# Performance work log

Measured on AMD Instinct MI355X. Metric: run time of the kernel, lower is better.

## Reference

```python
import jax, jax.numpy as jnp
import numpy as np

BN_EPS = 1e-5


def setup_inputs() -> dict:
    N, E, IND, HID = 50000, 800000, 128, 64
    key = jax.random.key(0)
    ks = jax.random.split(key, 4)
    x = jax.random.normal(ks[0], (N, IND), dtype=jnp.float32)
    edge_index = jax.random.randint(ks[1], (2, E), 0, N, dtype=jnp.int64)
    edge_attr = jax.random.normal(ks[2], (E, 1), dtype=jnp.float32)
    # Linear(indim, hiddendim, bias=False): weight [HID, IND]
    W = jax.random.normal(ks[3], (HID, IND), dtype=jnp.float32) * (1.0 / np.sqrt(IND))
    bias = jnp.zeros((HID,), dtype=jnp.float32)
    gamma = jnp.ones((HID,), dtype=jnp.float32)
    beta = jnp.zeros((HID,), dtype=jnp.float32)
    return {"x": x, "edge_index": edge_index, "edge_attr": edge_attr,
            "W": W, "bias": bias, "gamma": gamma, "beta": beta}


def reference(x, edge_index, edge_attr, W, bias, gamma, beta):
    N = x.shape[0]
    # add_self_loops
    loop = jnp.arange(N, dtype=edge_index.dtype)
    row = jnp.concatenate([edge_index[0], loop])  # source nodes
    col = jnp.concatenate([edge_index[1], loop])  # target nodes
    # linear (no bias)
    h = x @ W.T  # [N, HID]
    # symmetric GCN normalization: deg computed over col (targets)
    deg = jax.ops.segment_sum(jnp.ones_like(col, dtype=h.dtype), col, num_segments=N)
    deg_inv_sqrt = jnp.where(deg > 0, jax.lax.rsqrt(jnp.maximum(deg, 1.0)), 0.0)
    norm = deg_inv_sqrt[row] * deg_inv_sqrt[col]  # [E+N]
    # gather-scale-scatter: message x_j = h[row], aggregate (add) at col
    msg = norm[:, None] * h[row]                   # [E+N, HID]
    out = jax.ops.segment_sum(msg, col, num_segments=N)  # [N, HID]
    out = jax.nn.relu(out + bias)
    # BatchNorm1d (training mode: batch statistics, biased variance)
    mean = out.mean(axis=0)
    var = out.var(axis=0)
    return gamma * (out - mean) * jax.lax.rsqrt(var + BN_EPS) + beta
```

## Files before the change

kernel.cpp:

```cpp
#include <hip/hip_runtime.h>

constexpr int IND = 128;
constexpr int HID = 64;
constexpr int STRIDE = 64;
constexpr int BSHIFT = 7;
constexpr int BNODES = 128;
constexpr int NBMAX = 512;
constexpr int BCAP = 2560;
constexpr int CH = 4096;
constexpr int EPT = CH / 256;
constexpr int GB = 2048;
constexpr int RB = 64;
constexpr float BN_EPS = 1e-5f;

static inline size_t align256(size_t x) { return (x + 255) & ~(size_t)255; }

__device__ inline ushort f2bf(float f) {
  uint u = __float_as_uint(f);
  uint r = (u + 0x7FFFu + ((u >> 16) & 1u)) >> 16;
  return (ushort)r;
}
__device__ inline float bf2f(ushort u) {
  return __uint_as_float(((uint)u) << 16);
}

__global__ __launch_bounds__(256) void k_init(int* __restrict__ gCursor,
                                              int* __restrict__ cnt,
                                              uint* __restrict__ hrow, int N) {
  int i = threadIdx.x;
  gCursor[i] = 0;
  gCursor[i + 256] = 0;
  if (i == 0) cnt[N] = 0;
  if (i < 32) hrow[i] = 0;
}

__global__ __launch_bounds__(256) void k_fusedA(
    const float* __restrict__ x, const float* __restrict__ W,
    const int* __restrict__ col, const int* __restrict__ row,
    int* __restrict__ gCursor, uint* __restrict__ gBuf,
    ushort* __restrict__ h, int N, int E, int PARTB) {
  __shared__ float ws[IND * HID];
  int tid = threadIdx.x;
  if ((int)blockIdx.x < PARTB) {
    int* hist = (int*)ws;
    int* gbase = hist + NBMAX;
    for (int i = tid; i < NBMAX; i += 256) hist[i] = 0;
    __syncthreads();
    uint pay_[EPT];
    int b_[EPT];
    int r_[EPT];
    int bs = blockIdx.x * CH;
    const int4* col4 = (const int4*)(col + bs);
    const int4* row4 = (const int4*)(row + bs);
    int rem = E - bs;
#pragma unroll
    for (int j = 0; j < EPT / 4; ++j) {
      int i4 = j * 256 + tid;
      int base = i4 << 2;
      if (base < rem) {
        int4 c = col4[i4];
        int4 r = row4[i4];
        int cc[4] = {c.x, c.y, c.z, c.w};
        int rr[4] = {r.x, r.y, r.z, r.w};
#pragma unroll
        for (int t = 0; t < 4; ++t) {
          int jj = j * 4 + t;
          if (base + t < rem) {
            int b = cc[t] >> BSHIFT;
            b_[jj] = b;
            pay_[jj] = ((uint)(cc[t] & (BNODES - 1)) << 16) | (uint)rr[t];
            r_[jj] = atomicAdd(&hist[b], 1);
          } else {
            b_[jj] = -1;
          }
        }
      } else {
#pragma unroll
        for (int t = 0; t < 4; ++t) b_[j * 4 + t] = -1;
      }
    }
    __syncthreads();
    for (int i = tid; i < NBMAX; i += 256) {
      int hcnt = hist[i];
      gbase[i] = (hcnt > 0) ? atomicAdd(&gCursor[i], hcnt) : 0;
    }
    __syncthreads();
#pragma unroll
    for (int j = 0; j < EPT; ++j) {
      if (b_[j] >= 0) {
        int pos = gbase[b_[j]] + r_[j];
        if (pos >= 0 && pos < BCAP) gBuf[(size_t)b_[j] * BCAP + pos] = pay_[j];
      }
    }
  } else {
    int nb = (blockIdx.x - PARTB) * 64;
    for (int id = tid; id < 2048; id += 256) {
      int c = id & 63;
      int k4 = (id >> 6) << 2;
      float4 w = *(const float4*)&W[c * IND + k4];
      ws[(k4 + 0) * HID + c] = w.x;
      ws[(k4 + 1) * HID + c] = w.y;
      ws[(k4 + 2) * HID + c] = w.z;
      ws[(k4 + 3) * HID + c] = w.w;
    }
    __syncthreads();
    const int c0 = (tid & 15) << 2;
    const int n0 = (tid >> 4) << 2;
    const float* xr[4];
#pragma unroll
    for (int j = 0; j < 4; ++j) {
      int node = nb + n0 + j;
      if (node > N - 1) node = N - 1;
      xr[j] = x + (size_t)node * IND;
    }
    float acc[4][4] = {};
    for (int k = 0; k < IND; k += 4) {
      float4 xv0 = *(const float4*)(xr[0] + k);
      float4 xv1 = *(const float4*)(xr[1] + k);
      float4 xv2 = *(const float4*)(xr[2] + k);
      float4 xv3 = *(const float4*)(xr[3] + k);
      float4 w0 = *(const float4*)&ws[(k + 0) * HID + c0];
      float4 w1 = *(const float4*)&ws[(k + 1) * HID + c0];
      float4 w2 = *(const float4*)&ws[(k + 2) * HID + c0];
      float4 w3 = *(const float4*)&ws[(k + 3) * HID + c0];
      acc[0][0] += xv0.x * w0.x + xv0.y * w1.x + xv0.z * w2.x + xv0.w * w3.x;
      acc[0][1] += xv0.x * w0.y + xv0.y * w1.y + xv0.z * w2.y + xv0.w * w3.y;
      acc[0][2] += xv0.x * w0.z + xv0.y * w1.z + xv0.z * w2.z + xv0.w * w3.z;
      acc[0][3] += xv0.x * w0.w + xv0.y * w1.w + xv0.z * w2.w + xv0.w * w3.w;
      acc[1][0] += xv1.x * w0.x + xv1.y * w1.x + xv1.z * w2.x + xv1.w * w3.x;
      acc[1][1] += xv1.x * w0.y + xv1.y * w1.y + xv1.z * w2.y + xv1.w * w3.y;
      acc[1][2] += xv1.x * w0.z + xv1.y * w1.z + xv1.z * w2.z + xv1.w * w3.z;
      acc[1][3] += xv1.x * w0.w + xv1.y * w1.w + xv1.z * w2.w + xv1.w * w3.w;
      acc[2][0] += xv2.x * w0.x + xv2.y * w1.x + xv2.z * w2.x + xv2.w * w3.x;
      acc[2][1] += xv2.x * w0.y + xv2.y * w1.y + xv2.z * w2.y + xv2.w * w3.y;
      acc[2][2] += xv2.x * w0.z + xv2.y * w1.z + xv2.z * w2.z + xv2.w * w3.z;
      acc[2][3] += xv2.x * w0.w + xv2.y * w1.w + xv2.z * w2.w + xv2.w * w3.w;
      acc[3][0] += xv3.x * w0.x + xv3.y * w1.x + xv3.z * w2.x + xv3.w * w3.x;
      acc[3][1] += xv3.x * w0.y + xv3.y * w1.y + xv3.z * w2.y + xv3.w * w3.y;
      acc[3][2] += xv3.x * w0.z + xv3.y * w1.z + xv3.z * w2.z + xv3.w * w3.z;
      acc[3][3] += xv3.x * w0.w + xv3.y * w1.w + xv3.z * w2.w + xv3.w * w3.w;
    }
#pragma unroll
    for (int j = 0; j < 4; ++j) {
      int node = nb + n0 + j;
      if (node < N) {
        ushort4 o;
        o.x = f2bf(acc[j][0]);
        o.y = f2bf(acc[j][1]);
        o.z = f2bf(acc[j][2]);
        o.w = f2bf(acc[j][3]);
        *(ushort4*)&h[(size_t)node * HID + c0] = o;
      }
    }
  }
}

__global__ __launch_bounds__(256) void k_place2(const int* __restrict__ gCursor,
                                                const uint* __restrict__ gBuf,
                                                int* __restrict__ cnt,
                                                ushort* __restrict__ pack,
                                                ushort* __restrict__ h, int N,
                                                uint dummy) {
  __shared__ ushort spack[BNODES * STRIDE];
  __shared__ int scnt[BNODES];
  int tid = threadIdx.x;
  int b = blockIdx.x;
  int node0 = b << BSHIFT;
  uint dd = dummy | (dummy << 16);
  uint4 dv = make_uint4(dd, dd, dd, dd);
  uint4* sp4 = (uint4*)spack;
  for (int i = tid; i < BNODES * STRIDE / 8; i += 256) sp4[i] = dv;
  if (tid < BNODES) scnt[tid] = 0;
  __syncthreads();
  int m = gCursor[b];
  if (m > BCAP) m = BCAP;
  if (m < 0) m = 0;
  const uint* gb = gBuf + (size_t)b * BCAP;
  for (int i = tid; i < m; i += 256) {
    uint pay = gb[i];
    int dL = (int)(pay >> 16);
    ushort src = (ushort)(pay & 0xFFFFu);
    int k = atomicAdd(&scnt[dL], 1);
    if (k < STRIDE) spack[(dL << 6) + k] = src;
  }
  __syncthreads();
  int lim = N - node0;
  if (lim > BNODES) lim = BNODES;
  if (lim <= 0) return;
  uint4* gp4 = (uint4*)(pack + ((size_t)node0 << 6));
  int n4 = lim * (STRIDE / 8);
  for (int i = tid; i < n4; i += 256) gp4[i] = sp4[i];
  for (int j = tid; j < lim; j += 256) cnt[node0 + j] = scnt[j];
  uint4* h4 = (uint4*)(h + ((size_t)node0 << 6));
  int hn = lim * 8;
  for (int i = tid; i < hn; i += 256) {
    int node = i >> 3;
    float dis = rsqrtf((float)scnt[node] + 1.0f);
    uint4 v = h4[i];
    uint r0 = (uint)f2bf(dis * bf2f((ushort)(v.x & 0xffff))) |
              ((uint)f2bf(dis * bf2f((ushort)(v.x >> 16))) << 16);
    uint r1 = (uint)f2bf(dis * bf2f((ushort)(v.y & 0xffff))) |
              ((uint)f2bf(dis * bf2f((ushort)(v.y >> 16))) << 16);
    uint r2 = (uint)f2bf(dis * bf2f((ushort)(v.z & 0xffff))) |
              ((uint)f2bf(dis * bf2f((ushort)(v.z >> 16))) << 16);
    uint r3 = (uint)f2bf(dis * bf2f((ushort)(v.w & 0xffff))) |
              ((uint)f2bf(dis * bf2f((ushort)(v.w >> 16))) << 16);
    h4[i] = make_uint4(r0, r1, r2, r3);
  }
}

__global__ __launch_bounds__(256) void k_gather(const int* __restrict__ cnt,
                                                const ushort* __restrict__ pack,
                                                const ushort* __restrict__ h,
                                                const float* __restrict__ bias,
                                                ushort* __restrict__ ybf,
                                                float* __restrict__ partials,
                                                int N) {
  __shared__ float ls[4][64];
  __shared__ float lq[4][64];
  int tid = threadIdx.x;
  int lane = tid & 63;
  int wv = tid >> 6;
  int gw = blockIdx.x * 4 + wv;
  const int GW = GB * 4;
  float bs = bias[lane];
  float sacc = 0.f, qacc = 0.f;
  for (int wid = gw; wid < N; wid += GW) {
    int cw = __builtin_amdgcn_readfirstlane(cnt[wid]);
    int deg = cw < STRIDE ? cw : STRIDE;
    int pend = (deg + 7) & ~7;
    const ushort* pk = pack + ((size_t)wid << 6);
    float dc = rsqrtf((float)cw + 1.0f);
    float a0 = bf2f(h[(size_t)wid * HID + lane]);
    float a1 = 0.f, a2 = 0.f, a3 = 0.f;
    for (int j = 0; j < pend; j += 8) {
      uint4 pv = *(const uint4*)&pk[j];
      int s0 = (int)(pv.x & 0xffffu), s1 = (int)(pv.x >> 16);
      int s2 = (int)(pv.y & 0xffffu), s3 = (int)(pv.y >> 16);
      int s4 = (int)(pv.z & 0xffffu), s5 = (int)(pv.z >> 16);
      int s6 = (int)(pv.w & 0xffffu), s7 = (int)(pv.w >> 16);
      a0 += bf2f(h[(size_t)s0 * HID + lane]);
      a1 += bf2f(h[(size_t)s1 * HID + lane]);
      a2 += bf2f(h[(size_t)s2 * HID + lane]);
      a3 += bf2f(h[(size_t)s3 * HID + lane]);
      a0 += bf2f(h[(size_t)s4 * HID + lane]);
      a1 += bf2f(h[(size_t)s5 * HID + lane]);
      a2 += bf2f(h[(size_t)s6 * HID + lane]);
      a3 += bf2f(h[(size_t)s7 * HID + lane]);
    }
    float acc = (a0 + a1) + (a2 + a3);
    float y = fmaxf(dc * acc + bs, 0.f);
    ushort yb = f2bf(y);
    ybf[(size_t)wid * HID + lane] = yb;
    float yr = bf2f(yb);
    sacc += yr;
    qacc += yr * yr;
  }
  ls[wv][lane] = sacc;
  lq[wv][lane] = qacc;
  __syncthreads();
  if (tid < 64) {
    float ss = ls[0][tid] + ls[1][tid] + ls[2][tid] + ls[3][tid];
    float qq = lq[0][tid] + lq[1][tid] + lq[2][tid] + lq[3][tid];
    partials[blockIdx.x * 128 + tid] = ss;
    partials[blockIdx.x * 128 + 64 + tid] = qq;
  }
}

__global__ __launch_bounds__(256) void k_reduce(const float* __restrict__ partials,
                                                float* __restrict__ red1) {
  __shared__ float tmp[256];
  int tid = threadIdx.x;
  int c = tid & 127;
  int half = tid >> 7;
  const int PER = GB / RB;
  const int hb = PER / 2;
  int base = blockIdx.x * PER + half * hb;
  float s = 0.f;
  for (int b = base; b < base + hb; ++b) s += partials[b * 128 + c];
  tmp[tid] = s;
  __syncthreads();
  if (tid < 128) red1[blockIdx.x * 128 + tid] = tmp[tid] + tmp[tid + 128];
}

__global__ __launch_bounds__(256) void k_finalize(const ushort* __restrict__ y,
                                                  const float* __restrict__ red1,
                                                  const float* __restrict__ gamma,
                                                  const float* __restrict__ beta,
                                                  float* __restrict__ out,
                                                  float invN, int total8) {
  __shared__ float tmp[256];
  __shared__ float red[128];
  int tid = threadIdx.x;
  {
    int c = tid & 127;
    int half = tid >> 7;
    const int hb = RB / 2;
    float s = 0.f;
    for (int b = half * hb; b < (half + 1) * hb; ++b) s += red1[b * 128 + c];
    tmp[tid] = s;
    __syncthreads();
    if (tid < 128) red[tid] = tmp[tid] + tmp[tid + 128];
    __syncthreads();
  }
  int c0 = (tid & 7) << 3;
  float sc[8], sh[8];
#pragma unroll
  for (int k = 0; k < 8; ++k) {
    int c = c0 + k;
    float mean = red[c] * invN;
    float var = red[64 + c] * invN - mean * mean;
    float istd = rsqrtf(var + BN_EPS);
    float gm = gamma[c] * istd;
    sc[k] = gm;
    sh[k] = beta[c] - mean * gm;
  }
  int start = blockIdx.x * 256 + tid;
  int stride = gridDim.x * 256;
  for (int i = start; i < total8; i += stride) {
    uint4 v = *(const uint4*)&y[(size_t)i * 8];
    float f0 = bf2f((ushort)(v.x & 0xffff)), f1 = bf2f((ushort)(v.x >> 16));
    float f2 = bf2f((ushort)(v.y & 0xffff)), f3 = bf2f((ushort)(v.y >> 16));
    float f4 = bf2f((ushort)(v.z & 0xffff)), f5 = bf2f((ushort)(v.z >> 16));
    float f6 = bf2f((ushort)(v.w & 0xffff)), f7 = bf2f((ushort)(v.w >> 16));
    float4 o0 = make_float4(f0 * sc[0] + sh[0], f1 * sc[1] + sh[1],
                            f2 * sc[2] + sh[2], f3 * sc[3] + sh[3]);
    float4 o1 = make_float4(f4 * sc[4] + sh[4], f5 * sc[5] + sh[5],
                            f6 * sc[6] + sh[6], f7 * sc[7] + sh[7]);
    *(float4*)&out[(size_t)i * 8] = o0;
    *(float4*)&out[(size_t)i * 8 + 4] = o1;
  }
}

extern "C" void kernel_launch(void* const* d_in, const int* in_sizes, int n_in,
                              void* d_out, int out_size, void* d_ws, size_t ws_size,
                              hipStream_t stream) {
  const float* x = (const float*)d_in[0];
  const int* ei = (const int*)d_in[1];
  const float* W = (const float*)d_in[3];
  const float* bias = (const float*)d_in[4];
  const float* gamma = (const float*)d_in[5];
  const float* beta = (const float*)d_in[6];
  const int N = in_sizes[0] / IND;
  const int E = in_sizes[1] / 2;
  const int* rowp = ei;
  const int* colp = ei + E;
  float* out = (float*)d_out;

  const int NBUCK = (N + BNODES - 1) / BNODES;

  char* wsb = (char*)d_ws;
  size_t off = 0;
  int* cnt = (int*)(wsb + off);          off = align256(off + (size_t)(N + 1) * 4);
  int* gCursor = (int*)(wsb + off);      off = align256(off + (size_t)NBMAX * 4);
  float* partials = (float*)(wsb + off); off = align256(off + (size_t)GB * 128 * 4);
  float* red1 = (float*)(wsb + off);     off = align256(off + (size_t)RB * 128 * 4);
  ushort* h = (ushort*)(wsb + off);      off = align256(off + (size_t)(N + 1) * HID * 2);
  ushort* ybf = (ushort*)(wsb + off);    off = align256(off + (size_t)N * HID * 2);
  ushort* pack = (ushort*)(wsb + off);   off = align256(off + (size_t)N * STRIDE * 2);
  uint* gBuf = (uint*)(wsb + off);       off = align256(off + (size_t)NBUCK * BCAP * 4);

  const int PARTB = (E + CH - 1) / CH;
  const int MMB = (N + 63) / 64;

  k_init<<<1, 256, 0, stream>>>(gCursor, cnt, (uint*)(h + (size_t)N * HID), N);
  k_fusedA<<<PARTB + MMB, 256, 0, stream>>>(x, W, colp, rowp, gCursor, gBuf, h,
                                            N, E, PARTB);
  k_place2<<<NBUCK, 256, 0, stream>>>(gCursor, gBuf, cnt, pack, h, N, (uint)N);
  k_gather<<<GB, 256, 0, stream>>>(cnt, pack, h, bias, ybf, partials, N);
  k_reduce<<<RB, 256, 0, stream>>>(partials, red1);
  int total8 = N * (HID / 8);
  k_finalize<<<256, 256, 0, stream>>>(ybf, red1, gamma, beta, out,
                                      1.0f / (float)N, total8);
}
```

Baseline: 76.73 us.

## Fuse gather, BN reduction and finalize into one cooperative kernel

Replaces the separate gather, reduce and finalize launches with a single cooperative kernel. Each wave keeps its 25 per-node activations in registers, and two grid-wide syncs split the batch-norm statistics reduction. This removes two kernel launches and the bf16 round trip of the intermediate activations through global memory. In exchange it runs fewer concurrent waves for the latency-bound gather, pays for two grid barriers, and falls back to the old three-kernel path if the cooperative launch is not possible.

```diff
diff --git a/kernel.cpp b/kernel.cpp
--- a/kernel.cpp
+++ b/kernel.cpp
@@ -1,4 +1,5 @@
 #include <hip/hip_runtime.h>
+#include <hip/hip_cooperative_groups.h>
 
 constexpr int IND = 128;
 constexpr int HID = 64;
@@ -11,6 +12,8 @@
 constexpr int EPT = CH / 256;
 constexpr int GB = 2048;
 constexpr int RB = 64;
+constexpr int GB2 = 512;
+constexpr int YMAX = 25;
 constexpr float BN_EPS = 1e-5f;
 
 static inline size_t align256(size_t x) { return (x + 255) & ~(size_t)255; }
@@ -206,6 +209,95 @@
     uint r3 = (uint)f2bf(dis * bf2f((ushort)(v.w & 0xffff))) |
               ((uint)f2bf(dis * bf2f((ushort)(v.w >> 16))) << 16);
     h4[i] = make_uint4(r0, r1, r2, r3);
+  }
+}
+
+__global__ __launch_bounds__(256, 4) void k_gfin(
+    const int* __restrict__ cnt, const ushort* __restrict__ pack,
+    const ushort* __restrict__ h, const float* __restrict__ bias,
+    const float* __restrict__ gamma, const float* __restrict__ beta,
+    float* __restrict__ partials, float* __restrict__ red1,
+    float* __restrict__ out, int N, float invN) {
+  __shared__ float ls[4][64];
+  __shared__ float lq[4][64];
+  int tid = threadIdx.x;
+  int lane = tid & 63;
+  int wv = tid >> 6;
+  int gw = blockIdx.x * 4 + wv;
+  const int GW = GB2 * 4;
+  float bs = bias[lane];
+  float ys[YMAX];
+  float sacc = 0.f, qacc = 0.f;
+#pragma unroll
+  for (int k = 0; k < YMAX; ++k) {
+    int wid = gw + k * GW;
+    float y = 0.f;
+    if (wid < N) {
+      int cw = __builtin_amdgcn_readfirstlane(cnt[wid]);
+      int deg = cw < STRIDE ? cw : STRIDE;
+      int pend = (deg + 7) & ~7;
+      const ushort* pk = pack + ((size_t)wid << 6);
+      float dc = rsqrtf((float)cw + 1.0f);
+      float a0 = bf2f(h[(size_t)wid * HID + lane]);
+      float a1 = 0.f, a2 = 0.f, a3 = 0.f;
+      for (int j = 0; j < pend; j += 8) {
+        uint4 pv = *(const uint4*)&pk[j];
+        int s0 = (int)(pv.x & 0xffffu), s1 = (int)(pv.x >> 16);
+        int s2 = (int)(pv.y & 0xffffu), s3 = (int)(pv.y >> 16);
+        int s4 = (int)(pv.z & 0xffffu), s5 = (int)(pv.z >> 16);
+        int s6 = (int)(pv.w & 0xffffu), s7 = (int)(pv.w >> 16);
+        a0 += bf2f(h[(size_t)s0 * HID + lane]);
+        a1 += bf2f(h[(size_t)s1 * HID + lane]);
+        a2 += bf2f(h[(size_t)s2 * HID + lane]);
+        a3 += bf2f(h[(size_t)s3 * HID + lane]);
+        a0 += bf2f(h[(size_t)s4 * HID + lane]);
+        a1 += bf2f(h[(size_t)s5 * HID + lane]);
+        a2 += bf2f(h[(size_t)s6 * HID + lane]);
+        a3 += bf2f(h[(size_t)s7 * HID + lane]);
+      }
+      float acc = (a0 + a1) + (a2 + a3);
+      y = fmaxf(dc * acc + bs, 0.f);
+      sacc += y;
+      qacc += y * y;
+    }
+    ys[k] = y;
+  }
+  ls[wv][lane] = sacc;
+  lq[wv][lane] = qacc;
+  __syncthreads();
+  if (tid < 64) {
+    float ss = ls[0][tid] + ls[1][tid] + ls[2][tid] + ls[3][tid];
+    float qq = lq[0][tid] + lq[1][tid] + lq[2][tid] + lq[3][tid];
+    partials[blockIdx.x * 128 + tid] = ss;
+    partials[blockIdx.x * 128 + 64 + tid] = qq;
+  }
+  cooperative_groups::this_grid().sync();
+  if ((int)blockIdx.x < 64) {
+    float* tmp = &ls[0][0];
+    int c = tid & 127;
+    int half = tid >> 7;
+    int base = blockIdx.x * 8 + half * 4;
+    float s = 0.f;
+    for (int b = base; b < base + 4; ++b) s += partials[b * 128 + c];
+    tmp[tid] = s;
+    __syncthreads();
+    if (tid < 128) red1[blockIdx.x * 128 + tid] = tmp[tid] + tmp[tid + 128];
+  }
+  cooperative_groups::this_grid().sync();
+  float s = 0.f, q = 0.f;
+  for (int b = 0; b < 64; ++b) {
+    s += red1[b * 128 + lane];
+    q += red1[b * 128 + 64 + lane];
+  }
+  float mean = s * invN;
+  float var = q * invN - mean * mean;
+  float istd = rsqrtf(var + BN_EPS);
+  float gm = gamma[lane] * istd;
+  float sh = beta[lane] - mean * gm;
+#pragma unroll
+  for (int k = 0; k < YMAX; ++k) {
+    int wid = gw + k * GW;
+    if (wid < N) out[(size_t)wid * HID + lane] = ys[k] * gm + sh;
   }
 }
 
@@ -367,9 +459,31 @@
   k_fusedA<<<PARTB + MMB, 256, 0, stream>>>(x, W, colp, rowp, gCursor, gBuf, h,
                                             N, E, PARTB);
   k_place2<<<NBUCK, 256, 0, stream>>>(gCursor, gBuf, cnt, pack, h, N, (uint)N);
-  k_gather<<<GB, 256, 0, stream>>>(cnt, pack, h, bias, ybf, partials, N);
-  k_reduce<<<RB, 256, 0, stream>>>(partials, red1);
-  int total8 = N * (HID / 8);
-  k_finalize<<<256, 256, 0, stream>>>(ybf, red1, gamma, beta, out,
-                                      1.0f / (float)N, total8);
-}
+
+  int maxB = 0;
+  hipError_t oe = hipOccupancyMaxActiveBlocksPerMultiprocessor(
+      &maxB, (const void*)k_gfin, 256, 0);
+  bool useCoop = (oe == hipSuccess) && (maxB * 256 >= GB2) &&
+                 (N <= GB2 * 4 * YMAX);
+  bool coopDone = false;
+  if (useCoop) {
+    int Nv = N;
+    float invN = 1.0f / (float)N;
+    const int* cnt_c = cnt;
+    const ushort* pack_c = pack;
+    const ushort* h_c = h;
+    void* args[] = {(void*)&cnt_c, (void*)&pack_c, (void*)&h_c, (void*)&bias,
+                    (void*)&gamma, (void*)&beta, (void*)&partials, (void*)&red1,
+                    (void*)&out, (void*)&Nv, (void*)&invN};
+    hipError_t le = hipLaunchCooperativeKernel((const void*)k_gfin, dim3(GB2),
+                                               dim3(256), args, 0, stream);
+    coopDone = (le == hipSuccess);
+  }
+  if (!coopDone) {
+    k_gather<<<GB, 256, 0, stream>>>(cnt, pack, h, bias, ybf, partials, N);
+    k_reduce<<<RB, 256, 0, stream>>>(partials, red1);
+    int total8 = N * (HID / 8);
+    k_finalize<<<256, 256, 0, stream>>>(ybf, red1, gamma, beta, out,
+                                        1.0f / (float)N, total8);
+  }
+}
```

Measured after the change: 224.1 us. +192.1%, slower.
